# Optimization experiments

Hardware: AMD Instinct MI355X
Metric: run time of the kernel (lower is better)

## Reference

```python
import jax, jax.numpy as jnp
import numpy as np

L_MODES = 64
GRID = 128
OUT_GRID = 128
CIN = 64
COUT = 64
T_DIM = 256


def legendre_table(L, theta):
    """Fully-normalized associated Legendre P_bar_l^m(cos(theta)), Condon-Shortley.
    Returns (L, 2L-1, n_theta) with m indexed -(L-1)..(L-1) at axis 1."""
    nt = theta.shape[0]
    x = np.cos(theta)
    s = np.sin(theta)
    P = np.zeros((L, L, nt))
    P[0, 0] = np.sqrt(1.0 / (4.0 * np.pi))
    for m in range(1, L):
        P[m, m] = -np.sqrt((2.0 * m + 1.0) / (2.0 * m)) * s * P[m - 1, m - 1]
    for m in range(L - 1):
        P[m + 1, m] = np.sqrt(2.0 * m + 3.0) * x * P[m, m]
    for m in range(L):
        for l in range(m + 2, L):
            a = np.sqrt((4.0 * l * l - 1.0) / (l * l - m * m))
            b = np.sqrt(((l - 1.0) ** 2 - m * m) / (4.0 * (l - 1.0) ** 2 - 1.0))
            P[l, m] = a * (x * P[l - 1, m] - b * P[l - 2, m])
    T = np.zeros((L, 2 * L - 1, nt))
    for m in range(L):
        T[:, L - 1 + m, :] = P[:, m, :]
        if m > 0:
            T[:, L - 1 - m, :] = ((-1.0) ** m) * P[:, m, :]
    return T.astype(np.float32)


def setup_inputs() -> dict:
    key = jax.random.key(0)
    ks = jax.random.split(key, 8)
    theta = np.pi * (np.arange(GRID) + 0.5) / GRID
    theta_out = np.pi * (np.arange(OUT_GRID) + 0.5) / OUT_GRID
    P_in = jnp.asarray(legendre_table(L_MODES, theta))            # (L, 2L-1, GRID)
    P_out = jnp.asarray(legendre_table(L_MODES, theta_out))       # (L, 2L-1, OUT_GRID)
    quad_w = jnp.asarray((np.pi / GRID) * np.sin(theta), dtype=jnp.float32)
    scale_w = 1.0 / (CIN + COUT)
    return {
        "x": jax.random.normal(ks[0], (GRID, GRID, CIN), jnp.float32),
        "t_emb": jax.random.normal(ks[1], (T_DIM,), jnp.float32),
        "wr": scale_w * jax.random.normal(ks[2], (L_MODES, 2 * L_MODES - 1, CIN, COUT), jnp.float32),
        "wi": scale_w * jax.random.normal(ks[3], (L_MODES, 2 * L_MODES - 1, CIN, COUT), jnp.float32),
        "conv_w": jax.random.normal(ks[4], (CIN, COUT), jnp.float32) / np.sqrt(CIN),
        "conv_b": jnp.zeros((COUT,), jnp.float32),
        "time_w": jax.random.normal(ks[5], (COUT, COUT), jnp.float32),
        "dense_w": jax.random.normal(ks[6], (T_DIM, 2 * COUT), jnp.float32) / np.sqrt(T_DIM),
        "ln_scale": jnp.ones((COUT,), jnp.float32),
        "ln_bias": jnp.zeros((COUT,), jnp.float32),
        "P_in": P_in,
        "P_out": P_out,
        "quad_w": quad_w,
    }


def reference(x, t_emb, wr, wi, conv_w, conv_b, time_w, dense_w, ln_scale, ln_bias, P_in, P_out, quad_w):
    L = P_in.shape[0]
    G_out = P_out.shape[2]
    nlon = x.shape[1]
    m_idx = np.arange(-(L - 1), L)

    # ---- forward spherical harmonic transform (lon FFT + Legendre quadrature) ----
    f = jnp.fft.fft(x.astype(jnp.complex64), axis=1) * (2.0 * np.pi / nlon)  # (nlat, nlon, Cin)
    fm = f[:, np.mod(m_idx, nlon), :] * quad_w[:, None, None]                # (nlat, 2L-1, Cin)
    flm = jnp.einsum('tmc,lmt->lmc', fm, P_in)                                # (L, 2L-1, Cin)

    # ---- per-(l,m) complex spectral conv ----
    w = wr + 1j * wi
    flm = jnp.einsum('lmi,lmio->lmo', flm, w)                                 # (L, 2L-1, Cout)

    # ---- inverse SHT onto output grid ----
    g = jnp.einsum('lmo,lmt->tmo', flm, P_out)                                # (G_out, 2L-1, Cout)
    phi = 2.0 * np.pi * np.arange(G_out) / G_out
    E = jnp.asarray(np.exp(1j * np.outer(m_idx, phi)).astype(np.complex64))   # (2L-1, G_out)
    x_spec = jnp.real(jnp.einsum('tmo,mk->tko', g, E))                        # (G_out, G_out, Cout)

    # ---- residual time-conditioned path (TimeConv2D, einsum as written in source) ----
    h = jnp.einsum('lmk,ko->lmo', x, conv_w) + conv_b                          # 1x1 conv
    psi = t_emb @ dense_w
    w_t, b_t = jnp.split(psi, 2, axis=-1)
    h = jnp.einsum('ij,j,lmk->lmi', time_w, w_t, h) + b_t[None, None, :]
    h = jax.image.resize(h, (G_out, G_out, h.shape[-1]), method='bicubic')

    # ---- add, layernorm over channels, relu ----
    out = x_spec + h
    mu = jnp.mean(out, axis=-1, keepdims=True)
    var = jnp.var(out, axis=-1, keepdims=True)
    out = (out - mu) * jax.lax.rsqrt(var + 1e-6) * ln_scale + ln_bias
    return jax.nn.relu(out)
```

## Files before the change

### kernel.cpp

```cpp
#include <hip/hip_runtime.h>
#include <math.h>

#define LM 64
#define MM 127
#define GG 128
#define CC 64
#define OO 64

#define TWO_PI 6.28318530717958647692f

__global__ void k_pre(const float* __restrict__ t_emb, const float* __restrict__ dense_w,
                      const float* __restrict__ time_w, const float* __restrict__ conv_w,
                      const float* __restrict__ conv_b, float* __restrict__ aux) {
    __shared__ float psis[128];
    int j = threadIdx.x;
    float acc = 0.f;
    for (int t = 0; t < 256; ++t) acc += t_emb[t] * dense_w[t * 128 + j];
    psis[j] = acc;
    aux[j] = acc;
    __syncthreads();
    if (j < 64) {
        float tv = 0.f;
        for (int q = 0; q < 64; ++q) tv += time_w[j * 64 + q] * psis[q];
        aux[128 + j] = tv;
        float cs = 0.f;
        for (int o = 0; o < 64; ++o) cs += conv_w[j * 64 + o];
        aux[192 + j] = cs;
        if (j == 0) {
            float bs = 0.f;
            for (int o = 0; o < 64; ++o) bs += conv_b[o];
            aux[256] = bs;
        }
    }
}

__global__ __launch_bounds__(512) void k_dft(const float* __restrict__ x,
                                             const float* __restrict__ quad_w,
                                             float2* __restrict__ F) {
    __shared__ __align__(16) float smem[64 * 65 * 2];
    __shared__ float2 tab[GG];
    int t = blockIdx.x;
    int tx = threadIdx.x;
    int k = tx & 63, cg = tx >> 6;
    int c0 = cg * 8;

    float* xs = smem;
    {
        const float4* xp = (const float4*)(x + (size_t)t * GG * CC);
        float4* xd = (float4*)xs;
        for (int idx = tx; idx < GG * CC / 4; idx += 512) xd[idx] = xp[idx];
    }
    if (tx < GG) {
        float ang = (TWO_PI / GG) * tx;
        tab[tx] = make_float2(cosf(ang), sinf(ang));
    }
    __syncthreads();

    float sr[8], si[8];
#pragma unroll
    for (int j = 0; j < 8; ++j) { sr[j] = 0.f; si[j] = 0.f; }

    int kn = 0;
    for (int n = 0; n < GG; ++n) {
        float2 w = tab[kn];
        const float4 v0 = *(const float4*)&xs[n * 64 + c0];
        const float4 v1 = *(const float4*)&xs[n * 64 + c0 + 4];
        float vv[8] = {v0.x, v0.y, v0.z, v0.w, v1.x, v1.y, v1.z, v1.w};
#pragma unroll
        for (int j = 0; j < 8; ++j) {
            sr[j] += vv[j] * w.x;
            si[j] -= vv[j] * w.y;
        }
        kn = (kn + k) & (GG - 1);
    }
    float sc = (TWO_PI / GG) * quad_w[t];

    __syncthreads();
    float2* Fbuf = (float2*)smem;
#pragma unroll
    for (int j = 0; j < 8; ++j)
        Fbuf[k * 65 + c0 + j] = make_float2(sr[j] * sc, si[j] * sc);
    __syncthreads();
    float2* Fo = F + (size_t)t * 64 * CC;
    for (int idx = tx; idx < 64 * CC; idx += 512) {
        int kk = idx >> 6, cc = idx & 63;
        Fo[kk * CC + cc] = Fbuf[kk * 65 + cc];
    }
}

__global__ __launch_bounds__(128) void k_conv(const float* __restrict__ x,
                                              const float* __restrict__ aux,
                                              float* __restrict__ Sv) {
    __shared__ float xs[GG * 65];
    __shared__ float cws[CC];
    int t = blockIdx.x, tx = threadIdx.x;
    for (int idx = tx; idx < GG * CC; idx += 128) {
        int kk = idx >> 6, cc = idx & 63;
        xs[kk * 65 + cc] = x[((size_t)t * GG + kk) * CC + cc];
    }
    if (tx < 64) cws[tx] = aux[192 + tx];
    __syncthreads();
    float S = aux[256];
    for (int c = 0; c < CC; ++c) S += xs[tx * 65 + c] * cws[c];
    Sv[t * GG + tx] = S;
}

__global__ __launch_bounds__(256) void k_leg_fwd(const float2* __restrict__ F,
                                                 const float* __restrict__ P_in,
                                                 float2* __restrict__ flm) {
    int m = blockIdx.x;
    int lh = blockIdx.y;
    int l0 = lh * 32;
    if (l0 + 31 < m) return;

    __shared__ __align__(16) float2 Fs[64 * 64];
    __shared__ __align__(16) float  Ps[128 * 36];
    int tx = threadIdx.x;
    int c = tx & 63, lg = tx >> 6;

    for (int idx = tx; idx < 32 * 128; idx += 256) {
        int lr = idx >> 7, t = idx & 127;
        Ps[t * 36 + lr] = P_in[((size_t)(l0 + lr) * MM + 63 + m) * GG + t];
    }

    float sr[8], si[8];
#pragma unroll
    for (int j = 0; j < 8; ++j) { sr[j] = 0.f; si[j] = 0.f; }

    for (int tp = 0; tp < 2; ++tp) {
        __syncthreads();
        for (int idx = tx; idx < 64 * 64; idx += 256) {
            int tl = idx >> 6, cc = idx & 63;
            Fs[idx] = F[((size_t)(tp * 64 + tl) * 64 + m) * CC + cc];
        }
        __syncthreads();
        for (int tl = 0; tl < 64; ++tl) {
            int t = tp * 64 + tl;
            float2 f = Fs[tl * 64 + c];
            const float* pp = &Ps[t * 36 + lg * 8];
            float4 p0 = *(const float4*)pp;
            float4 p1 = *(const float4*)(pp + 4);
            float pv[8] = {p0.x, p0.y, p0.z, p0.w, p1.x, p1.y, p1.z, p1.w};
#pragma unroll
            for (int j = 0; j < 8; ++j) {
                sr[j] += f.x * pv[j];
                si[j] += f.y * pv[j];
            }
        }
    }
#pragma unroll
    for (int j = 0; j < 8; ++j) {
        int l = l0 + lg * 8 + j;
        if (l >= m) flm[((size_t)l * 64 + m) * CC + c] = make_float2(sr[j], si[j]);
    }
}

__global__ __launch_bounds__(256) void k_wmul(const float2* __restrict__ flm,
                                              const float* __restrict__ wr,
                                              const float* __restrict__ wi,
                                              float2* __restrict__ flm2) {
    int l = blockIdx.x, mi = blockIdx.y;
    int m = mi - 63;
    int am = m < 0 ? -m : m;
    if (l < am) return;
    __shared__ float2 fs[CC];
    __shared__ float2 part[4][CC];
    int tx = threadIdx.x, o = tx & 63, ig = tx >> 6;
    if (tx < 64) {
        float2 f = flm[((size_t)l * 64 + am) * CC + tx];
        if (m < 0) {
            float sgn = (am & 1) ? -1.f : 1.f;
            f.x *= sgn;
            f.y *= -sgn;
        }
        fs[tx] = f;
    }
    __syncthreads();
    size_t base = ((size_t)(l * MM + mi) * CC) * OO;
    const float* wrp = wr + base + o;
    const float* wip = wi + base + o;
    float ar = 0.f, ai = 0.f;
#pragma unroll
    for (int ii = 0; ii < 16; ++ii) {
        int i = ig * 16 + ii;
        float a = wrp[(size_t)i * OO];
        float b = wip[(size_t)i * OO];
        float2 f = fs[i];
        ar += f.x * a - f.y * b;
        ai += f.x * b + f.y * a;
    }
    part[ig][o] = make_float2(ar, ai);
    __syncthreads();
    if (tx < 64) {
        float2 r0 = part[0][tx], r1 = part[1][tx], r2 = part[2][tx], r3 = part[3][tx];
        flm2[(size_t)(l * MM + mi) * OO + tx] =
            make_float2(r0.x + r1.x + r2.x + r3.x, r0.y + r1.y + r2.y + r3.y);
    }
}

__global__ __launch_bounds__(256) void k_leg_inv(const float2* __restrict__ flm2,
                                                 const float* __restrict__ P_out,
                                                 float2* __restrict__ g) {
    int mi = blockIdx.x;
    int th = blockIdx.y >> 1, oh = blockIdx.y & 1;
    int t0 = th * 64, o0 = oh * 32;

    __shared__ __align__(16) float2 Ws[64 * 32];
    __shared__ __align__(16) float  Ps[64 * 64];
    int tx = threadIdx.x;
    int ol = tx & 31, tg = tx >> 5;
    int o = o0 + ol;

    for (int idx = tx; idx < 64 * 32; idx += 256) {
        int ls = idx >> 5, oo = idx & 31;
        Ws[idx] = flm2[(size_t)(ls * MM + mi) * OO + o0 + oo];
    }
    for (int idx = tx; idx < 64 * 64; idx += 256) {
        int ls = idx >> 6, tt = idx & 63;
        Ps[idx] = P_out[((size_t)ls * MM + mi) * GG + t0 + tt];
    }
    __syncthreads();

    float gr[8], gi[8];
#pragma unroll
    for (int j = 0; j < 8; ++j) { gr[j] = 0.f; gi[j] = 0.f; }

    for (int l = 0; l < 64; ++l) {
        float2 wv = Ws[l * 32 + ol];
        const float* pp = &Ps[l * 64 + tg * 8];
        float4 p0 = *(const float4*)pp;
        float4 p1 = *(const float4*)(pp + 4);
        float pv[8] = {p0.x, p0.y, p0.z, p0.w, p1.x, p1.y, p1.z, p1.w};
#pragma unroll
        for (int j = 0; j < 8; ++j) {
            gr[j] += wv.x * pv[j];
            gi[j] += wv.y * pv[j];
        }
    }
#pragma unroll
    for (int j = 0; j < 8; ++j) {
        int t = t0 + tg * 8 + j;
        g[((size_t)t * MM + mi) * OO + o] = make_float2(gr[j], gi[j]);
    }
}

__global__ __launch_bounds__(512) void k_final(const float2* __restrict__ g,
                                               const float* __restrict__ Sv,
                                               const float* __restrict__ aux,
                                               const float* __restrict__ ln_scale,
                                               const float* __restrict__ ln_bias,
                                               float* __restrict__ out) {
    __shared__ float2 gs[64 * 64];
    __shared__ float Ss[64];
    int t = blockIdx.x, kh = blockIdx.y;
    int tx = threadIdx.x;
    int o = tx & 63, kg = tx >> 6;

    if (tx < 64) Ss[tx] = Sv[t * GG + kh * 64 + tx];

    float zr[8], zi[8], accr[8], acci[8];
#pragma unroll
    for (int j = 0; j < 8; ++j) {
        int k = kh * 64 + kg * 8 + j;
        float phi = (TWO_PI / GG) * k;
        float s, c;
        __sincosf(phi, &s, &c);
        zr[j] = c; zi[j] = s;
        accr[j] = 0.f; acci[j] = 0.f;
    }

    for (int pass = 0; pass < 2; ++pass) {
        int mbase = (pass == 0) ? 64 : 0;
        int cnt = (pass == 0) ? 63 : 64;
        __syncthreads();
        for (int idx = tx; idx < cnt * 64; idx += 512) {
            int mm = idx >> 6, oo = idx & 63;
            gs[idx] = g[((size_t)t * MM + mbase + mm) * OO + oo];
        }
        __syncthreads();
        for (int mm = cnt - 1; mm >= 0; --mm) {
            float2 gv = gs[mm * 64 + o];
#pragma unroll
            for (int j = 0; j < 8; ++j) {
                float tr = accr[j] * zr[j] - acci[j] * zi[j] + gv.x;
                float ti = accr[j] * zi[j] + acci[j] * zr[j] + gv.y;
                accr[j] = tr; acci[j] = ti;
            }
        }
    }

    float tvec = aux[128 + o], bt = aux[64 + o];
    float lns = ln_scale[o], lnb = ln_bias[o];
#pragma unroll
    for (int j = 0; j < 8; ++j) {
        int k = kh * 64 + kg * 8 + j;
        float phi = (TWO_PI / GG) * k;
        float s63, c63;
        sincosf(63.f * phi, &s63, &c63);
        float xsp = accr[j] * c63 + acci[j] * s63;
        float val = xsp + tvec * Ss[k - kh * 64] + bt;

        float mu = val;
#pragma unroll
        for (int off = 1; off < 64; off <<= 1) mu += __shfl_xor(mu, off);
        mu *= (1.f / 64.f);
        float d = val - mu;
        float var = d * d;
#pragma unroll
        for (int off = 1; off < 64; off <<= 1) var += __shfl_xor(var, off);
        var *= (1.f / 64.f);
        float r = d * rsqrtf(var + 1e-6f) * lns + lnb;
        out[((size_t)(t * GG) + k) * OO + o] = fmaxf(r, 0.f);
    }
}

extern "C" void kernel_launch(void* const* d_in, const int* in_sizes, int n_in,
                              void* d_out, int out_size, void* d_ws, size_t ws_size,
                              hipStream_t stream) {
    const float* x        = (const float*)d_in[0];
    const float* t_emb    = (const float*)d_in[1];
    const float* wr       = (const float*)d_in[2];
    const float* wi       = (const float*)d_in[3];
    const float* conv_w   = (const float*)d_in[4];
    const float* conv_b   = (const float*)d_in[5];
    const float* time_w   = (const float*)d_in[6];
    const float* dense_w  = (const float*)d_in[7];
    const float* ln_scale = (const float*)d_in[8];
    const float* ln_bias  = (const float*)d_in[9];
    const float* P_in     = (const float*)d_in[10];
    const float* P_out    = (const float*)d_in[11];
    const float* quad_w   = (const float*)d_in[12];

    float* ws = (float*)d_ws;
    float*  aux  = ws;
    float2* F    = (float2*)(ws + 512);
    float2* flm  = (float2*)(ws + 1049088);
    float2* flm2 = (float2*)(ws + 1573376);
    float2* g    = (float2*)(ws + 2613760);
    float*  Sv   = ws + 4694528;

    float* out = (float*)d_out;

    k_pre<<<1, 128, 0, stream>>>(t_emb, dense_w, time_w, conv_w, conv_b, aux);
    k_dft<<<GG, 512, 0, stream>>>(x, quad_w, F);
    k_conv<<<GG, 128, 0, stream>>>(x, aux, Sv);
    k_leg_fwd<<<dim3(64, 2), 256, 0, stream>>>(F, P_in, flm);
    k_wmul<<<dim3(LM, MM), 256, 0, stream>>>(flm, wr, wi, flm2);
    k_leg_inv<<<dim3(MM, 4), 256, 0, stream>>>(flm2, P_out, g);
    k_final<<<dim3(GG, 2), 512, 0, stream>>>(g, Sv, aux, ln_scale, ln_bias, out);
}
```

Before: 364.8 us.

## Fuse prep, DFT and conv kernels; split DFT by channel halves; vectorize wmul loads

Merges k_pre, k_dft and k_conv into one launch. An extra block computes the time embedding, and each (row, channel-half) block does both the phi DFT and a partial channel reduction for the conv path, with the two partial sums added in k_final. The DFT now writes F directly with float4 stores and no shared-memory transpose, and runs twice as many smaller blocks. Separately, k_wmul loads weights as float4 with 16 partial sums per output instead of 4, aiming to improve bandwidth on the dominant weight stream.

Result: faster. 340.4 us (-6.7%).

```diff
diff --git a/kernel.cpp b/kernel.cpp
--- a/kernel.cpp
+++ b/kernel.cpp
@@ -9,52 +9,71 @@
 
 #define TWO_PI 6.28318530717958647692f
 
-__global__ void k_pre(const float* __restrict__ t_emb, const float* __restrict__ dense_w,
-                      const float* __restrict__ time_w, const float* __restrict__ conv_w,
-                      const float* __restrict__ conv_b, float* __restrict__ aux) {
-    __shared__ float psis[128];
-    int j = threadIdx.x;
-    float acc = 0.f;
-    for (int t = 0; t < 256; ++t) acc += t_emb[t] * dense_w[t * 128 + j];
-    psis[j] = acc;
-    aux[j] = acc;
-    __syncthreads();
-    if (j < 64) {
-        float tv = 0.f;
-        for (int q = 0; q < 64; ++q) tv += time_w[j * 64 + q] * psis[q];
-        aux[128 + j] = tv;
-        float cs = 0.f;
-        for (int o = 0; o < 64; ++o) cs += conv_w[j * 64 + o];
-        aux[192 + j] = cs;
-        if (j == 0) {
-            float bs = 0.f;
-            for (int o = 0; o < 64; ++o) bs += conv_b[o];
-            aux[256] = bs;
-        }
-    }
-}
-
-__global__ __launch_bounds__(512) void k_dft(const float* __restrict__ x,
+__global__ __launch_bounds__(256) void k_dft(const float* __restrict__ x,
                                              const float* __restrict__ quad_w,
-                                             float2* __restrict__ F) {
-    __shared__ __align__(16) float smem[64 * 65 * 2];
+                                             const float* __restrict__ conv_w,
+                                             const float* __restrict__ conv_b,
+                                             const float* __restrict__ t_emb,
+                                             const float* __restrict__ dense_w,
+                                             const float* __restrict__ time_w,
+                                             float2* __restrict__ F,
+                                             float* __restrict__ Sv,
+                                             float* __restrict__ aux) {
+    int b = blockIdx.x;
+    int tx = threadIdx.x;
+
+    if (b == 256) {
+        __shared__ float psis[128];
+        if (tx < 128) {
+            float acc = 0.f;
+            for (int tq = 0; tq < 256; ++tq) acc += t_emb[tq] * dense_w[tq * 128 + tx];
+            psis[tx] = acc;
+            aux[tx] = acc;
+        }
+        __syncthreads();
+        if (tx < 64) {
+            float tv = 0.f;
+            for (int q = 0; q < 64; ++q) tv += time_w[tx * 64 + q] * psis[q];
+            aux[128 + tx] = tv;
+        }
+        return;
+    }
+
+    int t = b >> 1, ch = b & 1;
+    int c0base = ch * 32;
+
+    __shared__ __align__(16) float xs[GG * 32];
     __shared__ float2 tab[GG];
-    int t = blockIdx.x;
-    int tx = threadIdx.x;
-    int k = tx & 63, cg = tx >> 6;
-    int c0 = cg * 8;
-
-    float* xs = smem;
+    __shared__ float cwsl[32];
+    __shared__ float Sp[2][GG];
+    __shared__ float bsum_s;
+
     {
-        const float4* xp = (const float4*)(x + (size_t)t * GG * CC);
-        float4* xd = (float4*)xs;
-        for (int idx = tx; idx < GG * CC / 4; idx += 512) xd[idx] = xp[idx];
+        const float* xp = x + (size_t)t * GG * CC + c0base;
+        for (int idx = tx; idx < GG * 32 / 4; idx += 256) {
+            int n = idx >> 3, cq = idx & 7;
+            *(float4*)&xs[n * 32 + cq * 4] = *(const float4*)&xp[n * CC + cq * 4];
+        }
     }
     if (tx < GG) {
         float ang = (TWO_PI / GG) * tx;
         tab[tx] = make_float2(cosf(ang), sinf(ang));
     }
-    __syncthreads();
+    if (tx >= 128 && tx < 160) {
+        int c = c0base + (tx - 128);
+        float s = 0.f;
+        for (int o = 0; o < OO; ++o) s += conv_w[c * OO + o];
+        cwsl[tx - 128] = s;
+    }
+    if (tx == 160) {
+        float bs = 0.f;
+        for (int o = 0; o < OO; ++o) bs += conv_b[o];
+        bsum_s = bs;
+    }
+    __syncthreads();
+
+    int k = tx & 63, cgl = tx >> 6;
+    int c0 = cgl * 8;
 
     float sr[8], si[8];
 #pragma unroll
@@ -63,8 +82,8 @@
     int kn = 0;
     for (int n = 0; n < GG; ++n) {
         float2 w = tab[kn];
-        const float4 v0 = *(const float4*)&xs[n * 64 + c0];
-        const float4 v1 = *(const float4*)&xs[n * 64 + c0 + 4];
+        const float4 v0 = *(const float4*)&xs[n * 32 + c0];
+        const float4 v1 = *(const float4*)&xs[n * 32 + c0 + 4];
         float vv[8] = {v0.x, v0.y, v0.z, v0.w, v1.x, v1.y, v1.z, v1.w};
 #pragma unroll
         for (int j = 0; j < 8; ++j) {
@@ -75,34 +94,28 @@
     }
     float sc = (TWO_PI / GG) * quad_w[t];
 
-    __syncthreads();
-    float2* Fbuf = (float2*)smem;
-#pragma unroll
-    for (int j = 0; j < 8; ++j)
-        Fbuf[k * 65 + c0 + j] = make_float2(sr[j] * sc, si[j] * sc);
-    __syncthreads();
-    float2* Fo = F + (size_t)t * 64 * CC;
-    for (int idx = tx; idx < 64 * CC; idx += 512) {
-        int kk = idx >> 6, cc = idx & 63;
-        Fo[kk * CC + cc] = Fbuf[kk * 65 + cc];
-    }
-}
-
-__global__ __launch_bounds__(128) void k_conv(const float* __restrict__ x,
-                                              const float* __restrict__ aux,
-                                              float* __restrict__ Sv) {
-    __shared__ float xs[GG * 65];
-    __shared__ float cws[CC];
-    int t = blockIdx.x, tx = threadIdx.x;
-    for (int idx = tx; idx < GG * CC; idx += 128) {
-        int kk = idx >> 6, cc = idx & 63;
-        xs[kk * 65 + cc] = x[((size_t)t * GG + kk) * CC + cc];
-    }
-    if (tx < 64) cws[tx] = aux[192 + tx];
-    __syncthreads();
-    float S = aux[256];
-    for (int c = 0; c < CC; ++c) S += xs[tx * 65 + c] * cws[c];
-    Sv[t * GG + tx] = S;
+    {
+        float2* Fp = F + ((size_t)t * 64 + k) * CC + c0base + c0;
+#pragma unroll
+        for (int q = 0; q < 4; ++q) {
+            float4 v = make_float4(sr[2 * q] * sc, si[2 * q] * sc,
+                                   sr[2 * q + 1] * sc, si[2 * q + 1] * sc);
+            *(float4*)&Fp[2 * q] = v;
+        }
+    }
+
+    {
+        int n2 = tx & 127, h = tx >> 7;
+        float p = 0.f;
+#pragma unroll
+        for (int j = 0; j < 16; ++j) p += xs[n2 * 32 + h * 16 + j] * cwsl[h * 16 + j];
+        Sp[h][n2] = p;
+    }
+    __syncthreads();
+    if (tx < GG) {
+        float v = Sp[0][tx] + Sp[1][tx] + (ch == 0 ? bsum_s : 0.f);
+        Sv[(size_t)ch * GG * GG + t * GG + tx] = v;
+    }
 }
 
 __global__ __launch_bounds__(256) void k_leg_fwd(const float2* __restrict__ F,
@@ -164,8 +177,8 @@
     int am = m < 0 ? -m : m;
     if (l < am) return;
     __shared__ float2 fs[CC];
-    __shared__ float2 part[4][CC];
-    int tx = threadIdx.x, o = tx & 63, ig = tx >> 6;
+    __shared__ float2 part[16][CC];
+    int tx = threadIdx.x, ol = tx & 15, ig = tx >> 4;
     if (tx < 64) {
         float2 f = flm[((size_t)l * 64 + am) * CC + tx];
         if (m < 0) {
@@ -177,24 +190,32 @@
     }
     __syncthreads();
     size_t base = ((size_t)(l * MM + mi) * CC) * OO;
-    const float* wrp = wr + base + o;
-    const float* wip = wi + base + o;
-    float ar = 0.f, ai = 0.f;
-#pragma unroll
-    for (int ii = 0; ii < 16; ++ii) {
-        int i = ig * 16 + ii;
-        float a = wrp[(size_t)i * OO];
-        float b = wip[(size_t)i * OO];
+    const float4* wr4 = (const float4*)(wr + base);
+    const float4* wi4 = (const float4*)(wi + base);
+    float ar[4] = {0.f, 0.f, 0.f, 0.f}, ai[4] = {0.f, 0.f, 0.f, 0.f};
+#pragma unroll
+    for (int di = 0; di < 4; ++di) {
+        int i = ig * 4 + di;
+        float4 a = wr4[i * 16 + ol];
+        float4 b = wi4[i * 16 + ol];
         float2 f = fs[i];
-        ar += f.x * a - f.y * b;
-        ai += f.x * b + f.y * a;
-    }
-    part[ig][o] = make_float2(ar, ai);
+        ar[0] += f.x * a.x - f.y * b.x;  ai[0] += f.x * b.x + f.y * a.x;
+        ar[1] += f.x * a.y - f.y * b.y;  ai[1] += f.x * b.y + f.y * a.y;
+        ar[2] += f.x * a.z - f.y * b.z;  ai[2] += f.x * b.z + f.y * a.z;
+        ar[3] += f.x * a.w - f.y * b.w;  ai[3] += f.x * b.w + f.y * a.w;
+    }
+#pragma unroll
+    for (int j = 0; j < 4; ++j) part[ig][ol * 4 + j] = make_float2(ar[j], ai[j]);
     __syncthreads();
     if (tx < 64) {
-        float2 r0 = part[0][tx], r1 = part[1][tx], r2 = part[2][tx], r3 = part[3][tx];
-        flm2[(size_t)(l * MM + mi) * OO + tx] =
-            make_float2(r0.x + r1.x + r2.x + r3.x, r0.y + r1.y + r2.y + r3.y);
+        float rr = 0.f, ri = 0.f;
+#pragma unroll
+        for (int q = 0; q < 16; ++q) {
+            float2 p = part[q][tx];
+            rr += p.x;
+            ri += p.y;
+        }
+        flm2[(size_t)(l * MM + mi) * OO + tx] = make_float2(rr, ri);
     }
 }
 
@@ -256,7 +277,8 @@
     int tx = threadIdx.x;
     int o = tx & 63, kg = tx >> 6;
 
-    if (tx < 64) Ss[tx] = Sv[t * GG + kh * 64 + tx];
+    if (tx < 64)
+        Ss[tx] = Sv[t * GG + kh * 64 + tx] + Sv[GG * GG + t * GG + kh * 64 + tx];
 
     float zr[8], zi[8], accr[8], acci[8];
 #pragma unroll
@@ -341,9 +363,8 @@
 
     float* out = (float*)d_out;
 
-    k_pre<<<1, 128, 0, stream>>>(t_emb, dense_w, time_w, conv_w, conv_b, aux);
-    k_dft<<<GG, 512, 0, stream>>>(x, quad_w, F);
-    k_conv<<<GG, 128, 0, stream>>>(x, aux, Sv);
+    k_dft<<<257, 256, 0, stream>>>(x, quad_w, conv_w, conv_b, t_emb, dense_w, time_w,
+                                   F, Sv, aux);
     k_leg_fwd<<<dim3(64, 2), 256, 0, stream>>>(F, P_in, flm);
     k_wmul<<<dim3(LM, MM), 256, 0, stream>>>(flm, wr, wi, flm2);
     k_leg_inv<<<dim3(MM, 4), 256, 0, stream>>>(flm2, P_out, g);
```
